# Kernel tuning notes

Hardware: AMD Instinct MI355X
Metric: run time of the kernel (lower is better)

The kernel has to match this reference:

```python
import jax, jax.numpy as jnp
import numpy as np

C, H, W = 32, 64, 64
KH, KW = 5, 5
OH, OW = 60, 60
N_IN = C * H * W
B, S = 64, 4096
CAP = 128


def _build_indices():
    # Enumerate every (c, kh, kw, oh, ow) slot of the unfold, matching
    # fold(unfold(order)) in the torch module (stride 1, pad 0, dilation 1).
    c = np.arange(C)[:, None, None, None, None]
    kh = np.arange(KH)[None, :, None, None, None]
    kw = np.arange(KW)[None, None, :, None, None]
    oh = np.arange(OH)[None, None, None, :, None]
    ow = np.arange(OW)[None, None, None, None, :]
    ids = c * (H * W) + (oh + kh) * W + (ow + kw)          # input flat id feeding slot
    ckk = c * (KH * KW) + kh * KW + kw                     # kernel-local channel index
    j = ckk * (OH * OW) + oh * OW + ow                     # flat slot in order_convoled
    ids, j = np.broadcast_arrays(ids, j)
    ids = ids.ravel().astype(np.int64)
    j = j.ravel().astype(np.int64)
    perm = np.argsort(ids, kind='stable')
    sid, sj = ids[perm], j[perm]
    counts = np.bincount(ids, minlength=N_IN)
    Lmax = int(counts.max())                               # = 25 here
    starts = np.concatenate([[0], np.cumsum(counts)[:-1]])
    rank = np.arange(sid.shape[0]) - starts[sid]
    indices = np.full((N_IN, Lmax), -1, dtype=np.int32)
    indices[sid, rank] = sj
    return indices


def setup_inputs() -> dict:
    key = jax.random.key(0)
    spikes = jax.random.randint(key, (B, S, 1, 1), 0, N_IN, dtype=jnp.int32)
    indices = jnp.asarray(_build_indices())
    return {"spikes": spikes, "indices": indices, "out_h": OH, "out_w": OW, "cap": CAP}


def reference(spikes, indices, out_h, out_w, cap):
    Bn, Sn = spikes.shape[0], spikes.shape[1]
    L = indices.shape[1]
    nbins = out_h * out_w
    E = Sn * L                                             # events per batch element

    ids = spikes[:, :, 0, 0]                               # [B,S] flat input ids
    g = indices[ids]                                       # [B,S,L] slots, -1 padded
    valid = g >= 0
    j = jnp.where(valid, g, 0)
    bins = (j % nbins).reshape(Bn * E)                     # output bin (oh*out_w+ow)
    ckk = (j // nbins).reshape(Bn * E)                     # kernel-local index to store
    valid_f = valid.reshape(Bn * E)
    b_idx = jnp.repeat(jnp.arange(Bn, dtype=jnp.int32), E)

    # Arrival-order rank within each (batch, bin): stable sort by global bin,
    # then rank = position - segment start (running max of change points).
    gbin = jnp.where(valid_f, b_idx * nbins + bins, Bn * nbins)   # sentinel for invalid
    perm = jnp.argsort(gbin)                               # stable
    sorted_gbin = gbin[perm]
    pos = jnp.arange(Bn * E, dtype=jnp.int32)
    change = jnp.concatenate([jnp.ones((1,), bool), sorted_gbin[1:] != sorted_gbin[:-1]])
    seg_start = jax.lax.cummax(jnp.where(change, pos, 0))
    rank_sorted = pos - seg_start
    rank = jnp.zeros(Bn * E, jnp.int32).at[perm].set(rank_sorted)  # inverse perm

    # Scatter ckk into per-bin slots; invalid / overflow events go to slot=cap (dropped).
    slot = jnp.where(valid_f & (rank < cap), rank, cap)
    out = jnp.full((Bn, cap + 1, nbins), -1, dtype=spikes.dtype)
    out = out.at[b_idx, slot, bins].set(jnp.where(valid_f, ckk, -1), mode='drop')
    return out[:, :cap].reshape(Bn, cap, out_h, out_w)
```

## Files before the change

kernel.cpp:

```cpp
#include <hip/hip_runtime.h>

#define OHh   60
#define OWw   60
#define NBINS (OHh * OWw)
#define NB    64
#define NS    4096
#define CAP   128

#define NW     4
#define SEG    (NS / NW)
#define CH     (SEG / 64)
#define HCAP   160
#define HBUF   176
#define PW     5
#define PRE0   64

__global__ __launch_bounds__(256) void sort_spikes_row4(
    const int* __restrict__ spikes, int* __restrict__ out) {
    const int bid  = (int)blockIdx.x;
    const int b    = bid & (NB - 1);
    const int row  = bid >> 6;
    const int tid  = (int)threadIdx.x;
    const int wv   = tid >> 6;
    const int lane = tid & 63;
    const bool valid = lane < OWw;

    __shared__ int            hitbuf[NW][HBUF];
    __shared__ unsigned       pres[NW][64][PW];
    __shared__ unsigned short outimg[PRE0][OWw];
    __shared__ int            cnt[NW][64];
    __shared__ int            ovf;

    const int* __restrict__ sp   = spikes + b * NS + wv * SEG;
    int* __restrict__       outb = out + (size_t)b * (CAP * NBINS) + row * OWw;

    int vs[CH];
#pragma unroll
    for (int c = 0; c < CH; ++c) vs[c] = sp[c * 64 + lane];

    if (tid == 0) ovf = 0;
#pragma unroll
    for (int i = 0; i < PW; ++i) pres[wv][lane][i] = 0u;
    {
        int* oi = (int*)&outimg[0][0];
        for (int i = tid; i < PRE0 * OWw / 2; i += 256) oi[i] = -1;
    }

    int* const hb_w = &hitbuf[wv][0];

    int hbase = 0;
#pragma unroll
    for (int c = 0; c < CH; ++c) {
        const int v = vs[c];
        const int h = (v >> 6) & 63;
        const int w = v & 63;
        const int A = (v >> 12) * 25 + h * 5 + w;
        const int R = (w << 16) | A;
        const bool halo = (unsigned)(h - row) < 5u;

        const unsigned long long mask = __ballot(halo);
        const int pos = __builtin_amdgcn_mbcnt_hi(
            (unsigned)(mask >> 32),
            __builtin_amdgcn_mbcnt_lo((unsigned)mask, 0));
        if (halo) hb_w[min(hbase + pos, HCAP - 1)] = R;
        hbase += (int)__popcll(mask);

        if (valid) outb[(PRE0 + wv * CH + c) * NBINS + lane] = -1;
    }
    if (hbase > HCAP && lane == 0) ovf = 1;
    const int n = min(hbase, HCAP);
    if (lane < 12) hb_w[n + lane] = 64 << 16;

    const int qi  = lane / 5;
    const int kwc = lane - qi * 5;
    for (int hbi = 0; hbi < n; hbi += 12) {
        const int hidx = hbi + qi;
        const int R    = hb_w[hidx];
        const int bin  = (R >> 16) - kwc;
        if ((unsigned)bin < 60u)
            atomicOr(&pres[wv][bin][hidx >> 5], 1u << (hidx & 31));
    }

    unsigned m0 = pres[wv][lane][0], m1 = pres[wv][lane][1];
    unsigned m2 = pres[wv][lane][2], m3 = pres[wv][lane][3];
    unsigned m4 = pres[wv][lane][4];
    cnt[wv][lane] = __builtin_popcount(m0) + __builtin_popcount(m1) +
                    __builtin_popcount(m2) + __builtin_popcount(m3) +
                    __builtin_popcount(m4);
    __syncthreads();

    if (ovf == 0) {
        if (valid) {
            int k = 0;
            for (int w = 0; w < wv; ++w) k += cnt[w][lane];
            const int sub = row * 5 + lane;
            unsigned mw[PW] = {m0, m1, m2, m3, m4};
#pragma unroll
            for (int wd = 0; wd < PW; ++wd) {
                unsigned mm = mw[wd];
                while (mm) {
                    const int j = __builtin_ctz(mm);
                    mm &= mm - 1;
                    const int src = wd * 32 + j;
                    const int ck  = (hb_w[src] & 0xffff) - sub;
                    if (k < PRE0) outimg[k][lane] = (unsigned short)ck;
                    else if (k < CAP) outb[k * NBINS + lane] = ck;
                    ++k;
                }
            }
        }
        __syncthreads();
        if (valid) {
#pragma unroll 4
            for (int i = 0; i < PRE0 / NW; ++i) {
                const int kk = wv * (PRE0 / NW) + i;
                outb[kk * NBINS + lane] = (int)(short)outimg[kk][lane];
            }
        }
    } else if (wv == 0) {
        const int* __restrict__ spf = spikes + b * NS;
        int cc = 0;
        for (int c = 0; c < NS / 64; ++c) {
            const int v = spf[c * 64 + lane];
            const int h = (v >> 6) & 63;
            unsigned long long mask = __ballot((unsigned)(h - row) < 5u);
            while (mask) {
                const int j = (int)__builtin_ctzll(mask);
                mask &= mask - 1;
                const int vj =
                    __builtin_amdgcn_readlane(v, __builtin_amdgcn_readfirstlane(j));
                const int wj  = vj & 63;
                const int khj = ((vj >> 6) & 63) - row;
                const int cj  = vj >> 12;
                const int kw  = wj - lane;
                if (((unsigned)kw < 5u) & valid) {
                    if (cc < CAP)
                        outb[cc * NBINS + lane] = cj * 25 + khj * 5 + kw;
                    ++cc;
                }
            }
        }
        if (valid)
            for (int k = cc; k < CAP; ++k) outb[k * NBINS + lane] = -1;
    }
}

extern "C" void kernel_launch(void* const* d_in, const int* in_sizes, int n_in,
                              void* d_out, int out_size, void* d_ws, size_t ws_size,
                              hipStream_t stream) {
    const int* spikes = (const int*)d_in[0];
    int* out = (int*)d_out;

    dim3 grid(OHh * NB);
    dim3 block(256);
    sort_spikes_row4<<<grid, block, 0, stream>>>(spikes, out);
}
```

Measured before the change: 138.6 us.

## Process two output rows per block with 512-thread blocks and smaller staging image

Each block now handles two output rows with eight waves, four per row, which halves the grid to 1920 blocks of 512 threads. The shared staging image shrinks from 64 to 48 slots per row, and the extra -1 fill writes for slots 48-63 are spread across the segment waves. This is meant to cut per-block launch and setup overhead and raise occupancy per CU. In exchange it uses more LDS per block, and more ranks may take the slower direct global-store path. The spike loads are not shared between the two rows; each wave still reloads its own segment.

```diff
diff --git a/kernel.cpp b/kernel.cpp
--- a/kernel.cpp
+++ b/kernel.cpp
@@ -7,31 +7,37 @@
 #define NS    4096
 #define CAP   128
 
-#define NW     4
-#define SEG    (NS / NW)
+#define NWPR   4
+#define RPB    2
+#define NW     (NWPR * RPB)
+#define RG     (OHh / RPB)
+#define SEG    (NS / NWPR)
 #define CH     (SEG / 64)
 #define HCAP   160
 #define HBUF   176
 #define PW     5
-#define PRE0   64
+#define PRE0   48
 
-__global__ __launch_bounds__(256) void sort_spikes_row4(
+__global__ __launch_bounds__(NW * 64) void sort_spikes_pair8(
     const int* __restrict__ spikes, int* __restrict__ out) {
     const int bid  = (int)blockIdx.x;
     const int b    = bid & (NB - 1);
-    const int row  = bid >> 6;
+    const int rg   = bid >> 6;
     const int tid  = (int)threadIdx.x;
     const int wv   = tid >> 6;
     const int lane = tid & 63;
     const bool valid = lane < OWw;
+    const int rsub = wv >> 2;
+    const int seg  = wv & 3;
+    const int row  = rg * RPB + rsub;
 
     __shared__ int            hitbuf[NW][HBUF];
     __shared__ unsigned       pres[NW][64][PW];
-    __shared__ unsigned short outimg[PRE0][OWw];
-    __shared__ int            cnt[NW][64];
+    __shared__ unsigned short outimg[RPB][PRE0][OWw];
+    __shared__ int            cnt[RPB][NWPR][64];
     __shared__ int            ovf;
 
-    const int* __restrict__ sp   = spikes + b * NS + wv * SEG;
+    const int* __restrict__ sp   = spikes + b * NS + seg * SEG;
     int* __restrict__       outb = out + (size_t)b * (CAP * NBINS) + row * OWw;
 
     int vs[CH];
@@ -42,8 +48,8 @@
 #pragma unroll
     for (int i = 0; i < PW; ++i) pres[wv][lane][i] = 0u;
     {
-        int* oi = (int*)&outimg[0][0];
-        for (int i = tid; i < PRE0 * OWw / 2; i += 256) oi[i] = -1;
+        int* oi = (int*)&outimg[0][0][0];
+        for (int i = tid; i < RPB * PRE0 * OWw / 2; i += NW * 64) oi[i] = -1;
     }
 
     int* const hb_w = &hitbuf[wv][0];
@@ -65,7 +71,12 @@
         if (halo) hb_w[min(hbase + pos, HCAP - 1)] = R;
         hbase += (int)__popcll(mask);
 
-        if (valid) outb[(PRE0 + wv * CH + c) * NBINS + lane] = -1;
+        if (valid) outb[(64 + seg * CH + c) * NBINS + lane] = -1;
+    }
+    if (valid) {
+#pragma unroll
+        for (int i = 0; i < 4; ++i)
+            outb[(PRE0 + seg * 4 + i) * NBINS + lane] = -1;
     }
     if (hbase > HCAP && lane == 0) ovf = 1;
     const int n = min(hbase, HCAP);
@@ -84,15 +95,15 @@
     unsigned m0 = pres[wv][lane][0], m1 = pres[wv][lane][1];
     unsigned m2 = pres[wv][lane][2], m3 = pres[wv][lane][3];
     unsigned m4 = pres[wv][lane][4];
-    cnt[wv][lane] = __builtin_popcount(m0) + __builtin_popcount(m1) +
-                    __builtin_popcount(m2) + __builtin_popcount(m3) +
-                    __builtin_popcount(m4);
+    cnt[rsub][seg][lane] = __builtin_popcount(m0) + __builtin_popcount(m1) +
+                           __builtin_popcount(m2) + __builtin_popcount(m3) +
+                           __builtin_popcount(m4);
     __syncthreads();
 
     if (ovf == 0) {
         if (valid) {
             int k = 0;
-            for (int w = 0; w < wv; ++w) k += cnt[w][lane];
+            for (int s = 0; s < seg; ++s) k += cnt[rsub][s][lane];
             const int sub = row * 5 + lane;
             unsigned mw[PW] = {m0, m1, m2, m3, m4};
 #pragma unroll
@@ -103,7 +114,7 @@
                     mm &= mm - 1;
                     const int src = wd * 32 + j;
                     const int ck  = (hb_w[src] & 0xffff) - sub;
-                    if (k < PRE0) outimg[k][lane] = (unsigned short)ck;
+                    if (k < PRE0) outimg[rsub][k][lane] = (unsigned short)ck;
                     else if (k < CAP) outb[k * NBINS + lane] = ck;
                     ++k;
                 }
@@ -112,12 +123,12 @@
         __syncthreads();
         if (valid) {
 #pragma unroll 4
-            for (int i = 0; i < PRE0 / NW; ++i) {
-                const int kk = wv * (PRE0 / NW) + i;
-                outb[kk * NBINS + lane] = (int)(short)outimg[kk][lane];
+            for (int i = 0; i < PRE0 / NWPR; ++i) {
+                const int kk = seg * (PRE0 / NWPR) + i;
+                outb[kk * NBINS + lane] = (int)(short)outimg[rsub][kk][lane];
             }
         }
-    } else if (wv == 0) {
+    } else if (seg == 0) {
         const int* __restrict__ spf = spikes + b * NS;
         int cc = 0;
         for (int c = 0; c < NS / 64; ++c) {
@@ -127,8 +138,8 @@
             while (mask) {
                 const int j = (int)__builtin_ctzll(mask);
                 mask &= mask - 1;
-                const int vj =
-                    __builtin_amdgcn_readlane(v, __builtin_amdgcn_readfirstlane(j));
+                const int vj = __builtin_amdgcn_readlane(
+                    v, __builtin_amdgcn_readfirstlane(j));
                 const int wj  = vj & 63;
                 const int khj = ((vj >> 6) & 63) - row;
                 const int cj  = vj >> 12;
@@ -151,7 +162,7 @@
     const int* spikes = (const int*)d_in[0];
     int* out = (int*)d_out;
 
-    dim3 grid(OHh * NB);
-    dim3 block(256);
-    sort_spikes_row4<<<grid, block, 0, stream>>>(spikes, out);
+    dim3 grid(RG * NB);
+    dim3 block(NW * 64);
+    sort_spikes_pair8<<<grid, block, 0, stream>>>(spikes, out);
 }
```

New measurement: 140.1 us. No clear change (+1.1%).
